# Optimization experiments

Hardware: AMD Instinct MI355X
Metric: run time of the kernel (lower is better)

Reference implementation:

```python
import jax, jax.numpy as jnp
import numpy as np

N_HEAD, D_K, D_V, D_MODEL = 16, 64, 64, 1024
LN_EPS = 1e-5


def setup_inputs() -> dict:
    key = jax.random.key(0)
    ks = jax.random.split(key, 13)
    B, S = 2, 2048
    s = 1.0 / np.sqrt(D_MODEL)
    return {
        "q": jax.random.normal(ks[0], (B, S, D_MODEL), jnp.float32),
        "k": jax.random.normal(ks[1], (B, S, D_MODEL), jnp.float32),
        "v": jax.random.normal(ks[2], (B, S, D_MODEL), jnp.float32),
        "Wq": jax.random.normal(ks[3], (D_MODEL, N_HEAD * D_K), jnp.float32) * s,
        "bq": jnp.zeros((N_HEAD * D_K,), jnp.float32),
        "Wk": jax.random.normal(ks[4], (D_MODEL, N_HEAD * D_K), jnp.float32) * s,
        "bk": jnp.zeros((N_HEAD * D_K,), jnp.float32),
        "Wv": jax.random.normal(ks[5], (D_MODEL, N_HEAD * D_V), jnp.float32) * s,
        "bv": jnp.zeros((N_HEAD * D_V,), jnp.float32),
        "Wo": jax.random.normal(ks[6], (N_HEAD * D_V, D_MODEL), jnp.float32) * s,
        "bo": jnp.zeros((D_MODEL,), jnp.float32),
        "ln_gamma": jnp.ones((D_MODEL,), jnp.float32),
        "ln_beta": jnp.zeros((D_MODEL,), jnp.float32),
    }


def reference(q, k, v, Wq, bq, Wk, bk, Wv, bv, Wo, bo, ln_gamma, ln_beta):
    B, S, _ = q.shape
    temperature = jnp.asarray(np.power(D_K, 0.5), q.dtype)
    # QKV projections -> [B, S, H, d]
    q_ = (q @ Wq + bq).reshape(B, S, N_HEAD, D_K)
    k_ = (k @ Wk + bk).reshape(B, S, N_HEAD, D_K)
    v_ = (v @ Wv + bv).reshape(B, S, N_HEAD, D_V)
    # scaled dot-product attention per head
    scores = jnp.einsum("bqhd,bkhd->bhqk", q_, k_) / temperature
    attn = jax.nn.softmax(scores, axis=-1)
    ctx = jnp.einsum("bhqk,bkhd->bqhd", attn, v_).reshape(B, S, N_HEAD * D_V)
    # output projection + residual + LayerNorm
    out = ctx @ Wo + bo + q
    mu = jnp.mean(out, axis=-1, keepdims=True)
    var = jnp.var(out, axis=-1, keepdims=True)
    out = (out - mu) * jax.lax.rsqrt(var + LN_EPS) * ln_gamma + ln_beta
    return out
```

## Files before the change

### kernel.cpp

```cpp
#include <hip/hip_runtime.h>
#include <hip/hip_bf16.h>

typedef float f32x4 __attribute__((ext_vector_type(4)));
typedef float f32x16 __attribute__((ext_vector_type(16)));
typedef __bf16 bf16x8 __attribute__((ext_vector_type(8)));
typedef __bf16 bf16x4 __attribute__((ext_vector_type(4)));
typedef unsigned u32x2 __attribute__((ext_vector_type(2)));

#define DM 1024
#define SL 2048
#define NHEAD 16
#define LOG2E 1.44269504088896f
#define EXP2(x) __builtin_amdgcn_exp2f(x)

static __device__ __forceinline__ f32x4 mfma16(bf16x8 a, bf16x8 b, f32x4 c) {
    return __builtin_amdgcn_mfma_f32_16x16x32_bf16(a, b, c, 0, 0, 0);
}
static __device__ __forceinline__ f32x16 mfma32(bf16x8 a, bf16x8 b, f32x16 c) {
    return __builtin_amdgcn_mfma_f32_32x32x16_bf16(a, b, c, 0, 0, 0);
}

static __device__ __forceinline__ void gload16(const void* g, void* l) {
    __builtin_amdgcn_global_load_lds(
        (const __attribute__((address_space(1))) unsigned*)g,
        (__attribute__((address_space(3))) unsigned*)l, 16, 0, 0);
}

static __device__ __forceinline__ unsigned packbf(float lo, float hi) {
    unsigned short lu = __builtin_bit_cast(unsigned short, (__bf16)lo);
    unsigned short hu = __builtin_bit_cast(unsigned short, (__bf16)hi);
    return ((unsigned)hu << 16) | (unsigned)lu;
}

__global__ __launch_bounds__(256) void cast_kernel(
    const float* __restrict__ x0, const float* __restrict__ x1, const float* __restrict__ x2,
    __bf16* __restrict__ y0, __bf16* __restrict__ y1, __bf16* __restrict__ y2)
{
    const float* x = (blockIdx.y == 0) ? x0 : (blockIdx.y == 1) ? x1 : x2;
    __bf16* y = (blockIdx.y == 0) ? y0 : (blockIdx.y == 1) ? y1 : y2;
    size_t i = ((size_t)blockIdx.x * 256 + threadIdx.x) * 8;
    float4 a = *reinterpret_cast<const float4*>(&x[i]);
    float4 b = *reinterpret_cast<const float4*>(&x[i + 4]);
    bf16x8 o;
    o[0] = (__bf16)a.x; o[1] = (__bf16)a.y; o[2] = (__bf16)a.z; o[3] = (__bf16)a.w;
    o[4] = (__bf16)b.x; o[5] = (__bf16)b.y; o[6] = (__bf16)b.z; o[7] = (__bf16)b.w;
    *reinterpret_cast<bf16x8*>(&y[i]) = o;
}

__global__ __launch_bounds__(256) void wt4_kernel(
    const float* __restrict__ W0, const float* __restrict__ W1,
    const float* __restrict__ W2, const float* __restrict__ W3,
    __bf16* __restrict__ T0, __bf16* __restrict__ T1,
    __bf16* __restrict__ T2, __bf16* __restrict__ T3)
{
    const float* W = (blockIdx.z == 0) ? W0 : (blockIdx.z == 1) ? W1
                   : (blockIdx.z == 2) ? W2 : W3;
    __bf16* Wt = (blockIdx.z == 0) ? T0 : (blockIdx.z == 1) ? T1
               : (blockIdx.z == 2) ? T2 : T3;
    __shared__ float tle[32][33];
    const int tx = threadIdx.x, ty = threadIdx.y;
    const int n0 = blockIdx.x * 32, k0 = blockIdx.y * 32;
#pragma unroll
    for (int i = 0; i < 4; ++i) {
        int r = ty + 8 * i;
        tle[r][tx] = W[(size_t)(k0 + r) * DM + (n0 + tx)];
    }
    __syncthreads();
#pragma unroll
    for (int i = 0; i < 4; ++i) {
        int r = ty + 8 * i;
        Wt[(size_t)(n0 + r) * DM + (k0 + tx)] = (__bf16)tle[tx][r];
    }
}

static __device__ __forceinline__ void gemm_body_bf16(
    const __bf16* __restrict__ A, const __bf16* __restrict__ Wt,
    const float* __restrict__ bias,
    __bf16* __restrict__ Yb,
    int mode, float oscale, int r0, int c0)
{
    __shared__ __attribute__((aligned(16))) __bf16 As[128 * 64];
    __shared__ __attribute__((aligned(16))) __bf16 Bs[128 * 64];
    const int t = threadIdx.x;
    const int w = t >> 6, lane = t & 63;
    const int l15 = lane & 15, lhi = lane >> 4;
    const int wr = w >> 1, wc = w & 1;
    const int lrow = lane >> 3;
    const int lcolswz = (((lane & 7) ^ lrow) << 3);
    const int jb = w * 4;
    const int swzr = (l15 & 7) << 3;

    const f32x4 fzero = {0.f, 0.f, 0.f, 0.f};
    f32x4 acc[4][4];
#pragma unroll
    for (int m = 0; m < 4; ++m)
#pragma unroll
        for (int n = 0; n < 4; ++n) acc[m][n] = fzero;

    const __bf16* gA = &A[(size_t)(r0 + jb * 8 + lrow) * DM + lcolswz];
    const __bf16* gB = &Wt[(size_t)(c0 + jb * 8 + lrow) * DM + lcolswz];

    for (int kt = 0; kt < DM; kt += 64) {
        __syncthreads();
#pragma unroll
        for (int i = 0; i < 4; ++i) {
            gload16(gA + (size_t)i * 8 * DM + kt, &As[(jb + i) * 512]);
            gload16(gB + (size_t)i * 8 * DM + kt, &Bs[(jb + i) * 512]);
        }
        __syncthreads();
#pragma unroll
        for (int kk = 0; kk < 2; ++kk) {
            bf16x8 af[4], bfr[4];
#pragma unroll
            for (int m = 0; m < 4; ++m)
                af[m] = *reinterpret_cast<const bf16x8*>(
                    &As[(wr * 64 + m * 16 + l15) * 64 + ((kk * 32 + lhi * 8) ^ swzr)]);
#pragma unroll
            for (int n = 0; n < 4; ++n)
                bfr[n] = *reinterpret_cast<const bf16x8*>(
                    &Bs[(wc * 64 + n * 16 + l15) * 64 + ((kk * 32 + lhi * 8) ^ swzr)]);
#pragma unroll
            for (int m = 0; m < 4; ++m)
#pragma unroll
                for (int n = 0; n < 4; ++n)
                    acc[m][n] = mfma16(af[m], bfr[n], acc[m][n]);
        }
    }
    if (mode == 0) {
#pragma unroll
        for (int m = 0; m < 4; ++m)
#pragma unroll
            for (int n = 0; n < 4; ++n)
#pragma unroll
                for (int r = 0; r < 4; ++r) {
                    int grow = r0 + wr * 64 + m * 16 + lhi * 4 + r;
                    int gcol = c0 + wc * 64 + n * 16 + l15;
                    Yb[(size_t)grow * DM + gcol] =
                        (__bf16)((acc[m][n][r] + bias[gcol]) * oscale);
                }
    } else {
#pragma unroll
        for (int m = 0; m < 4; ++m)
#pragma unroll
            for (int n = 0; n < 4; ++n) {
                int token = r0 + wr * 64 + m * 16 + lhi * 4;
                int gcol = c0 + wc * 64 + n * 16 + l15;
                int bb = token >> 11, ss = token & (SL - 1);
                int hh = gcol >> 6, dd = gcol & 63;
                float bv = bias[gcol];
                bf16x4 pv;
#pragma unroll
                for (int r = 0; r < 4; ++r) pv[r] = (__bf16)(acc[m][n][r] + bv);
                *reinterpret_cast<bf16x4*>(
                    &Yb[(((size_t)(bb * NHEAD + hh)) * 64 + dd) * SL + ss]) = pv;
            }
    }
}

__global__ __launch_bounds__(256) void qkv_kernel(
    const __bf16* __restrict__ xq, const __bf16* __restrict__ xk, const __bf16* __restrict__ xv,
    const __bf16* __restrict__ WtQ, const __bf16* __restrict__ WtK, const __bf16* __restrict__ WtV,
    const float* __restrict__ bq, const float* __restrict__ bk, const float* __restrict__ bv,
    __bf16* __restrict__ Qp, __bf16* __restrict__ Kp, __bf16* __restrict__ Vt)
{
    const int p = blockIdx.x;
    const int logical = (p & 7) * 96 + (p >> 3);
    const int x = logical & 7;
    const int s = logical >> 3;
    const int y = s & 31, z = s >> 5;
    const __bf16* X = (z == 0) ? xq : (z == 1) ? xk : xv;
    const __bf16* Wt = (z == 0) ? WtQ : (z == 1) ? WtK : WtV;
    const float* bias = (z == 0) ? bq : (z == 1) ? bk : bv;
    __bf16* Yb = (z == 0) ? Qp : (z == 1) ? Kp : Vt;
    int mode = (z == 2) ? 1 : 0;
    float oscale = (z == 0) ? (0.125f * LOG2E) : 1.0f;
    gemm_body_bf16(X, Wt, bias, Yb, mode, oscale, y * 128, x * 128);
}

__global__ __launch_bounds__(256) void oproj_kernel(
    const __bf16* __restrict__ Cxb, const __bf16* __restrict__ WtO,
    const float* __restrict__ bo, const float* __restrict__ resid,
    float* __restrict__ pre)
{
    __shared__ __attribute__((aligned(16))) __bf16 As[128 * 64];
    __shared__ __attribute__((aligned(16))) __bf16 Bs[64 * 64];
    const int p = blockIdx.x;
    const int logical = (p & 7) * 64 + (p >> 3);
    const int x = logical & 15, y = logical >> 4;
    const int r0 = y * 128, c0 = x * 64;

    const int t = threadIdx.x;
    const int w = t >> 6, lane = t & 63;
    const int l15 = lane & 15, lhi = lane >> 4;
    const int wr = w >> 1, wc = w & 1;
    const int lrow = lane >> 3;
    const int lcolswz = (((lane & 7) ^ lrow) << 3);
    const int jb = w * 4, jb2 = w * 2;
    const int swzr = (l15 & 7) << 3;

    const f32x4 fzero = {0.f, 0.f, 0.f, 0.f};
    f32x4 acc[4][2];
#pragma unroll
    for (int m = 0; m < 4; ++m)
#pragma unroll
        for (int n = 0; n < 2; ++n) acc[m][n] = fzero;

    const __bf16* gA = &Cxb[(size_t)(r0 + jb * 8 + lrow) * DM + lcolswz];
    const __bf16* gB = &WtO[(size_t)(c0 + jb2 * 8 + lrow) * DM + lcolswz];

    for (int kt = 0; kt < DM; kt += 64) {
        __syncthreads();
#pragma unroll
        for (int i = 0; i < 4; ++i)
            gload16(gA + (size_t)i * 8 * DM + kt, &As[(jb + i) * 512]);
#pragma unroll
        for (int i = 0; i < 2; ++i)
            gload16(gB + (size_t)i * 8 * DM + kt, &Bs[(jb2 + i) * 512]);
        __syncthreads();
#pragma unroll
        for (int kk = 0; kk < 2; ++kk) {
            bf16x8 af[4], bfr[2];
#pragma unroll
            for (int m = 0; m < 4; ++m)
                af[m] = *reinterpret_cast<const bf16x8*>(
                    &As[(wr * 64 + m * 16 + l15) * 64 + ((kk * 32 + lhi * 8) ^ swzr)]);
#pragma unroll
            for (int n = 0; n < 2; ++n)
                bfr[n] = *reinterpret_cast<const bf16x8*>(
                    &Bs[(wc * 32 + n * 16 + l15) * 64 + ((kk * 32 + lhi * 8) ^ swzr)]);
#pragma unroll
            for (int m = 0; m < 4; ++m)
#pragma unroll
                for (int n = 0; n < 2; ++n)
                    acc[m][n] = mfma16(af[m], bfr[n], acc[m][n]);
        }
    }
#pragma unroll
    for (int m = 0; m < 4; ++m)
#pragma unroll
        for (int n = 0; n < 2; ++n)
#pragma unroll
            for (int r = 0; r < 4; ++r) {
                int grow = r0 + wr * 64 + m * 16 + lhi * 4 + r;
                int gcol = c0 + wc * 32 + n * 16 + l15;
                size_t idx = (size_t)grow * DM + gcol;
                pre[idx] = acc[m][n][r] + bo[gcol] + resid[idx];
            }
}

__global__ __launch_bounds__(512, 4) void attn_kernel(
    const __bf16* __restrict__ Qp, const __bf16* __restrict__ Kp,
    const __bf16* __restrict__ Vt, __bf16* __restrict__ Op, float2* __restrict__ ML)
{
    __shared__ __attribute__((aligned(16))) __bf16 Kl[2][4096];
    __shared__ __attribute__((aligned(16))) __bf16 Vl[2][4096];
    const int t = threadIdx.x;
    const int w = t >> 6, lane = t & 63;
    const int l31 = lane & 31, hi = lane >> 5;

    const int id = blockIdx.x;
    const int logical = (id & 7) * 64 + (id >> 3);
    const int bh = logical >> 4, rr = logical & 15;
    const int qs = rr >> 1, half = rr & 1;
    const int b = bh >> 4, h = bh & 15;
    const size_t tokQ = (size_t)b * SL + qs * 256 + w * 32;
    const size_t kbase = (size_t)b * SL + half * 1024;
    const size_t vrow0 = (size_t)bh * 64;

    const int srow = t >> 3, scol = (t & 7) << 3;
    const __bf16* gK = &Kp[(kbase + srow) * DM + h * 64 + scol];
    const __bf16* gV = &Vt[(vrow0 + srow) * SL + half * 1024 + scol];
    const int sidx = ((srow * 128 + scol * 2) ^ ((srow & 7) << 4)) >> 1;

    bf16x8 bq[4];
#pragma unroll
    for (int ks = 0; ks < 4; ++ks)
        bq[ks] = *reinterpret_cast<const bf16x8*>(
            &Qp[(tokQ + l31) * DM + h * 64 + ks * 16 + hi * 8]);

    f32x16 o0, o1;
#pragma unroll
    for (int r = 0; r < 16; ++r) { o0[r] = 0.f; o1[r] = 0.f; }
    float m_run = -1e30f, l_run = 0.f;

    const int swz = (l31 & 7) << 4;
    const int NT = 1024 / 64;

    {
        bf16x8 kv = *reinterpret_cast<const bf16x8*>(gK);
        bf16x8 vv = *reinterpret_cast<const bf16x8*>(gV);
        *reinterpret_cast<bf16x8*>(&Kl[0][sidx]) = kv;
        *reinterpret_cast<bf16x8*>(&Vl[0][sidx]) = vv;
    }

    for (int ti = 0; ti < NT; ++ti) {
        const int cb = ti & 1;
        const bool pf = (ti + 1 < NT);
        bf16x8 kvn, vvn;
        if (pf) {
            kvn = *reinterpret_cast<const bf16x8*>(gK + (size_t)(ti + 1) * 64 * DM);
            vvn = *reinterpret_cast<const bf16x8*>(gV + (ti + 1) * 64);
        }
        __syncthreads();

        f32x16 c0, c1;
#pragma unroll
        for (int r = 0; r < 16; ++r) { c0[r] = 0.f; c1[r] = 0.f; }
        __builtin_amdgcn_s_setprio(1);
#pragma unroll
        for (int ks = 0; ks < 4; ++ks) {
            int off = ks * 32 + hi * 16;
            bf16x8 ak0 = *reinterpret_cast<const bf16x8*>(&Kl[cb][((l31 * 128 + off) ^ swz) >> 1]);
            bf16x8 ak1 = *reinterpret_cast<const bf16x8*>(&Kl[cb][(((32 + l31) * 128 + off) ^ swz) >> 1]);
            c0 = mfma32(ak0, bq[ks], c0);
            c1 = mfma32(ak1, bq[ks], c1);
        }
        __builtin_amdgcn_s_setprio(0);

        float mx[8];
#pragma unroll
        for (int r = 0; r < 8; ++r)
            mx[r] = fmaxf(fmaxf(c0[r], c0[r + 8]), fmaxf(c1[r], c1[r + 8]));
#pragma unroll
        for (int r = 0; r < 4; ++r) mx[r] = fmaxf(mx[r], mx[r + 4]);
        float tm = fmaxf(fmaxf(mx[0], mx[1]), fmaxf(mx[2], mx[3]));
        tm = fmaxf(tm, __shfl_xor(tm, 32));

        if (__any(tm > m_run + 11.5f)) {
            float nm = fmaxf(m_run, tm);
            float sc = EXP2(m_run - nm);
            m_run = nm;
            l_run *= sc;
#pragma unroll
            for (int r = 0; r < 16; ++r) {
                float sq = __shfl(sc, (r & 3) + 8 * (r >> 2) + 4 * hi);
                o0[r] *= sq; o1[r] *= sq;
            }
        }

        float s4a = 0.f, s4b = 0.f, s4c = 0.f, s4d = 0.f;
#pragma unroll
        for (int r = 0; r < 16; r += 4) {
            c0[r]     = EXP2(c0[r]     - m_run); s4a += c0[r];
            c0[r + 1] = EXP2(c0[r + 1] - m_run); s4b += c0[r + 1];
            c0[r + 2] = EXP2(c0[r + 2] - m_run); s4c += c0[r + 2];
            c0[r + 3] = EXP2(c0[r + 3] - m_run); s4d += c0[r + 3];
        }
#pragma unroll
        for (int r = 0; r < 16; r += 4) {
            c1[r]     = EXP2(c1[r]     - m_run); s4a += c1[r];
            c1[r + 1] = EXP2(c1[r + 1] - m_run); s4b += c1[r + 1];
            c1[r + 2] = EXP2(c1[r + 2] - m_run); s4c += c1[r + 2];
            c1[r + 3] = EXP2(c1[r + 3] - m_run); s4d += c1[r + 3];
        }
        float rs = (s4a + s4b) + (s4c + s4d);
        rs += __shfl_xor(rs, 32);
        l_run += rs;

        if (pf) {
            *reinterpret_cast<bf16x8*>(&Kl[cb ^ 1][sidx]) = kvn;
            *reinterpret_cast<bf16x8*>(&Vl[cb ^ 1][sidx]) = vvn;
        }

        unsigned wd0[8], wd1[8];
#pragma unroll
        for (int tt = 0; tt < 4; ++tt)
#pragma unroll
            for (int p = 0; p < 2; ++p) {
                wd0[tt * 2 + p] = packbf(c0[4 * tt + 2 * p], c0[4 * tt + 2 * p + 1]);
                wd1[tt * 2 + p] = packbf(c1[4 * tt + 2 * p], c1[4 * tt + 2 * p + 1]);
            }
        unsigned ua[4][4];
#pragma unroll
        for (int s = 0; s < 4; ++s) {
            int tA = (s & 1) * 2;
#pragma unroll
            for (int p = 0; p < 2; ++p) {
                unsigned va = (s < 2) ? wd0[tA * 2 + p] : wd1[tA * 2 + p];
                unsigned vb = (s < 2) ? wd0[(tA + 1) * 2 + p] : wd1[(tA + 1) * 2 + p];
                u32x2 rres = __builtin_amdgcn_permlane32_swap(va, vb, false, false);
                ua[s][p] = rres[0]; ua[s][2 + p] = rres[1];
            }
        }

        __builtin_amdgcn_s_setprio(1);
#pragma unroll
        for (int s = 0; s < 4; ++s) {
            bf16x8 as = *reinterpret_cast<const bf16x8*>(&ua[s][0]);
            bf16x8 vf0 = *reinterpret_cast<const bf16x8*>(
                &Vl[cb][((l31 * 128 + s * 32 + hi * 16) ^ swz) >> 1]);
            bf16x8 vf1 = *reinterpret_cast<const bf16x8*>(
                &Vl[cb][(((32 + l31) * 128 + s * 32 + hi * 16) ^ swz) >> 1]);
            o0 = mfma32(as, vf0, o0);
            o1 = mfma32(as, vf1, o1);
        }
        __builtin_amdgcn_s_setprio(0);
    }

    if (hi == 0)
        ML[((size_t)half * 4096 + tokQ + l31) * NHEAD + h] = float2{m_run, l_run};
    const size_t obase = (size_t)half * 4096 * DM;
#pragma unroll
    for (int r = 0; r < 16; ++r) {
        int qq = (r & 3) + 8 * (r >> 2) + 4 * hi;
        size_t rowi = obase + (tokQ + qq) * DM + h * 64;
        Op[rowi + l31]      = (__bf16)o0[r];
        Op[rowi + 32 + l31] = (__bf16)o1[r];
    }
}

__global__ __launch_bounds__(256) void combine_kernel(
    const __bf16* __restrict__ Op, const float2* __restrict__ ML,
    __bf16* __restrict__ Cxb)
{
    const size_t e = ((size_t)blockIdx.x * 256 + threadIdx.x) * 8;
    const int token = (int)(e >> 10);
    const int h = (int)((e >> 6) & 15);
    float2 ml0 = ML[(size_t)token * NHEAD + h];
    float2 ml1 = ML[((size_t)4096 + token) * NHEAD + h];
    float M = fmaxf(ml0.x, ml1.x);
    float s0 = EXP2(ml0.x - M), s1 = EXP2(ml1.x - M);
    float inv = 1.f / (ml0.y * s0 + ml1.y * s1);
    s0 *= inv; s1 *= inv;
    bf16x8 a0 = *reinterpret_cast<const bf16x8*>(&Op[e]);
    bf16x8 a1 = *reinterpret_cast<const bf16x8*>(&Op[(size_t)4096 * DM + e]);
    bf16x8 o;
#pragma unroll
    for (int j = 0; j < 8; ++j)
        o[j] = (__bf16)((float)a0[j] * s0 + (float)a1[j] * s1);
    *reinterpret_cast<bf16x8*>(&Cxb[e]) = o;
}

__global__ __launch_bounds__(256) void ln_kernel(
    const float* __restrict__ X, const float* __restrict__ gamma,
    const float* __restrict__ beta, float* __restrict__ out)
{
    const int row = blockIdx.x, t = threadIdx.x;
    float4 v = *reinterpret_cast<const float4*>(&X[(size_t)row * DM + t * 4]);
    float s = v.x + v.y + v.z + v.w;
    float s2 = v.x * v.x + v.y * v.y + v.z * v.z + v.w * v.w;
#pragma unroll
    for (int off = 1; off < 64; off <<= 1) {
        s += __shfl_xor(s, off);
        s2 += __shfl_xor(s2, off);
    }
    __shared__ float rs[4], rs2[4];
    const int w = t >> 6;
    if ((t & 63) == 0) { rs[w] = s; rs2[w] = s2; }
    __syncthreads();
    s = rs[0] + rs[1] + rs[2] + rs[3];
    s2 = rs2[0] + rs2[1] + rs2[2] + rs2[3];
    float mean = s * (1.f / DM);
    float var = s2 * (1.f / DM) - mean * mean;
    float rstd = rsqrtf(var + 1e-5f);
    int c = t * 4;
    float4 o;
    o.x = (v.x - mean) * rstd * gamma[c + 0] + beta[c + 0];
    o.y = (v.y - mean) * rstd * gamma[c + 1] + beta[c + 1];
    o.z = (v.z - mean) * rstd * gamma[c + 2] + beta[c + 2];
    o.w = (v.w - mean) * rstd * gamma[c + 3] + beta[c + 3];
    *reinterpret_cast<float4*>(&out[(size_t)row * DM + c]) = o;
}

extern "C" void kernel_launch(void* const* d_in, const int* in_sizes, int n_in,
                              void* d_out, int out_size, void* d_ws, size_t ws_size,
                              hipStream_t stream) {
    (void)in_sizes; (void)n_in; (void)out_size; (void)ws_size;
    const float* q   = (const float*)d_in[0];
    const float* k   = (const float*)d_in[1];
    const float* v   = (const float*)d_in[2];
    const float* Wq  = (const float*)d_in[3];
    const float* bq  = (const float*)d_in[4];
    const float* Wk  = (const float*)d_in[5];
    const float* bk  = (const float*)d_in[6];
    const float* Wv  = (const float*)d_in[7];
    const float* bv  = (const float*)d_in[8];
    const float* Wo  = (const float*)d_in[9];
    const float* bo  = (const float*)d_in[10];
    const float* lng = (const float*)d_in[11];
    const float* lnb = (const float*)d_in[12];

    char* ws = (char*)d_ws;
    const size_t MB = (size_t)1 << 20;
    __bf16* WtQ = (__bf16*)(ws + 0 * MB);
    __bf16* WtK = (__bf16*)(ws + 2 * MB);
    __bf16* WtV = (__bf16*)(ws + 4 * MB);
    __bf16* WtO = (__bf16*)(ws + 6 * MB);
    __bf16* Xbq = (__bf16*)(ws + 8 * MB);
    __bf16* Xbk = (__bf16*)(ws + 16 * MB);
    __bf16* Xbv = (__bf16*)(ws + 24 * MB);
    __bf16* Qp  = (__bf16*)(ws + 32 * MB);
    __bf16* Kp  = (__bf16*)(ws + 40 * MB);
    __bf16* Vt  = (__bf16*)(ws + 48 * MB);
    __bf16* Cxb = (__bf16*)(ws + 56 * MB);
    __bf16* Op  = (__bf16*)(ws + 8 * MB);
    float2* ML  = (float2*)(ws + 24 * MB);
    float*  pre = (float*)(ws + 8 * MB);

    cast_kernel<<<dim3(2048, 3), 256, 0, stream>>>(q, k, v, Xbq, Xbk, Xbv);
    wt4_kernel<<<dim3(32, 32, 4), dim3(32, 8), 0, stream>>>(
        Wq, Wk, Wv, Wo, WtQ, WtK, WtV, WtO);

    qkv_kernel<<<dim3(768), 256, 0, stream>>>(Xbq, Xbk, Xbv, WtQ, WtK, WtV,
                                              bq, bk, bv, Qp, Kp, Vt);
    attn_kernel<<<dim3(512), 512, 0, stream>>>(Qp, Kp, Vt, Op, ML);
    combine_kernel<<<dim3(2048), 256, 0, stream>>>(Op, ML, Cxb);
    oproj_kernel<<<dim3(512), 256, 0, stream>>>(Cxb, WtO, bo, q, pre);
    ln_kernel<<<4096, 256, 0, stream>>>(pre, lng, lnb, (float*)d_out);
}
```

Before: 147.6 us.

## Merge prep kernels, shrink QKV GEMM tiles, halve attention block size

Fuses the input cast and weight transpose into a single prep launch. The QKV projection now reuses the 128x64 GEMM body shared with the output projection, so it runs twice as many blocks. Attention blocks drop from 512 to 256 threads (128 query rows each), with every thread loading two K/V rows per tile, which doubles the grid to 1024 blocks. The aim is more blocks to fill the CUs and one fewer launch, at the cost of less operand reuse per block and more redundant K/V loading across blocks.

```diff
diff --git a/kernel.cpp b/kernel.cpp
--- a/kernel.cpp
+++ b/kernel.cpp
@@ -32,163 +32,57 @@
     return ((unsigned)hu << 16) | (unsigned)lu;
 }
 
-__global__ __launch_bounds__(256) void cast_kernel(
+__global__ __launch_bounds__(256) void prep_kernel(
     const float* __restrict__ x0, const float* __restrict__ x1, const float* __restrict__ x2,
-    __bf16* __restrict__ y0, __bf16* __restrict__ y1, __bf16* __restrict__ y2)
-{
-    const float* x = (blockIdx.y == 0) ? x0 : (blockIdx.y == 1) ? x1 : x2;
-    __bf16* y = (blockIdx.y == 0) ? y0 : (blockIdx.y == 1) ? y1 : y2;
-    size_t i = ((size_t)blockIdx.x * 256 + threadIdx.x) * 8;
-    float4 a = *reinterpret_cast<const float4*>(&x[i]);
-    float4 b = *reinterpret_cast<const float4*>(&x[i + 4]);
-    bf16x8 o;
-    o[0] = (__bf16)a.x; o[1] = (__bf16)a.y; o[2] = (__bf16)a.z; o[3] = (__bf16)a.w;
-    o[4] = (__bf16)b.x; o[5] = (__bf16)b.y; o[6] = (__bf16)b.z; o[7] = (__bf16)b.w;
-    *reinterpret_cast<bf16x8*>(&y[i]) = o;
-}
-
-__global__ __launch_bounds__(256) void wt4_kernel(
+    __bf16* __restrict__ y0, __bf16* __restrict__ y1, __bf16* __restrict__ y2,
     const float* __restrict__ W0, const float* __restrict__ W1,
     const float* __restrict__ W2, const float* __restrict__ W3,
     __bf16* __restrict__ T0, __bf16* __restrict__ T1,
     __bf16* __restrict__ T2, __bf16* __restrict__ T3)
 {
-    const float* W = (blockIdx.z == 0) ? W0 : (blockIdx.z == 1) ? W1
-                   : (blockIdx.z == 2) ? W2 : W3;
-    __bf16* Wt = (blockIdx.z == 0) ? T0 : (blockIdx.z == 1) ? T1
-               : (blockIdx.z == 2) ? T2 : T3;
-    __shared__ float tle[32][33];
-    const int tx = threadIdx.x, ty = threadIdx.y;
-    const int n0 = blockIdx.x * 32, k0 = blockIdx.y * 32;
-#pragma unroll
-    for (int i = 0; i < 4; ++i) {
-        int r = ty + 8 * i;
-        tle[r][tx] = W[(size_t)(k0 + r) * DM + (n0 + tx)];
-    }
-    __syncthreads();
-#pragma unroll
-    for (int i = 0; i < 4; ++i) {
-        int r = ty + 8 * i;
-        Wt[(size_t)(n0 + r) * DM + (k0 + tx)] = (__bf16)tle[tx][r];
-    }
-}
-
-static __device__ __forceinline__ void gemm_body_bf16(
+    const int bid = blockIdx.x;
+    if (bid < 6144) {
+        const int yy = bid >> 11, xx = bid & 2047;
+        const float* x = (yy == 0) ? x0 : (yy == 1) ? x1 : x2;
+        __bf16* y = (yy == 0) ? y0 : (yy == 1) ? y1 : y2;
+        size_t i = ((size_t)xx * 256 + threadIdx.x) * 8;
+        float4 a = *reinterpret_cast<const float4*>(&x[i]);
+        float4 b = *reinterpret_cast<const float4*>(&x[i + 4]);
+        bf16x8 o;
+        o[0] = (__bf16)a.x; o[1] = (__bf16)a.y; o[2] = (__bf16)a.z; o[3] = (__bf16)a.w;
+        o[4] = (__bf16)b.x; o[5] = (__bf16)b.y; o[6] = (__bf16)b.z; o[7] = (__bf16)b.w;
+        *reinterpret_cast<bf16x8*>(&y[i]) = o;
+    } else {
+        __shared__ float tle[32][33];
+        const int rem = bid - 6144;
+        const int z = rem >> 10, r2 = rem & 1023;
+        const int bx = r2 & 31, by = r2 >> 5;
+        const float* W = (z == 0) ? W0 : (z == 1) ? W1 : (z == 2) ? W2 : W3;
+        __bf16* Wt = (z == 0) ? T0 : (z == 1) ? T1 : (z == 2) ? T2 : T3;
+        const int tx = threadIdx.x & 31, ty = threadIdx.x >> 5;
+        const int n0 = bx * 32, k0 = by * 32;
+#pragma unroll
+        for (int i = 0; i < 4; ++i) {
+            int r = ty + 8 * i;
+            tle[r][tx] = W[(size_t)(k0 + r) * DM + (n0 + tx)];
+        }
+        __syncthreads();
+#pragma unroll
+        for (int i = 0; i < 4; ++i) {
+            int r = ty + 8 * i;
+            Wt[(size_t)(n0 + r) * DM + (k0 + tx)] = (__bf16)tle[tx][r];
+        }
+    }
+}
+
+static __device__ __forceinline__ void gemm64_body(
     const __bf16* __restrict__ A, const __bf16* __restrict__ Wt,
-    const float* __restrict__ bias,
-    __bf16* __restrict__ Yb,
+    const float* __restrict__ bias, const float* __restrict__ resid,
+    __bf16* __restrict__ Yb, float* __restrict__ Yf,
     int mode, float oscale, int r0, int c0)
-{
-    __shared__ __attribute__((aligned(16))) __bf16 As[128 * 64];
-    __shared__ __attribute__((aligned(16))) __bf16 Bs[128 * 64];
-    const int t = threadIdx.x;
-    const int w = t >> 6, lane = t & 63;
-    const int l15 = lane & 15, lhi = lane >> 4;
-    const int wr = w >> 1, wc = w & 1;
-    const int lrow = lane >> 3;
-    const int lcolswz = (((lane & 7) ^ lrow) << 3);
-    const int jb = w * 4;
-    const int swzr = (l15 & 7) << 3;
-
-    const f32x4 fzero = {0.f, 0.f, 0.f, 0.f};
-    f32x4 acc[4][4];
-#pragma unroll
-    for (int m = 0; m < 4; ++m)
-#pragma unroll
-        for (int n = 0; n < 4; ++n) acc[m][n] = fzero;
-
-    const __bf16* gA = &A[(size_t)(r0 + jb * 8 + lrow) * DM + lcolswz];
-    const __bf16* gB = &Wt[(size_t)(c0 + jb * 8 + lrow) * DM + lcolswz];
-
-    for (int kt = 0; kt < DM; kt += 64) {
-        __syncthreads();
-#pragma unroll
-        for (int i = 0; i < 4; ++i) {
-            gload16(gA + (size_t)i * 8 * DM + kt, &As[(jb + i) * 512]);
-            gload16(gB + (size_t)i * 8 * DM + kt, &Bs[(jb + i) * 512]);
-        }
-        __syncthreads();
-#pragma unroll
-        for (int kk = 0; kk < 2; ++kk) {
-            bf16x8 af[4], bfr[4];
-#pragma unroll
-            for (int m = 0; m < 4; ++m)
-                af[m] = *reinterpret_cast<const bf16x8*>(
-                    &As[(wr * 64 + m * 16 + l15) * 64 + ((kk * 32 + lhi * 8) ^ swzr)]);
-#pragma unroll
-            for (int n = 0; n < 4; ++n)
-                bfr[n] = *reinterpret_cast<const bf16x8*>(
-                    &Bs[(wc * 64 + n * 16 + l15) * 64 + ((kk * 32 + lhi * 8) ^ swzr)]);
-#pragma unroll
-            for (int m = 0; m < 4; ++m)
-#pragma unroll
-                for (int n = 0; n < 4; ++n)
-                    acc[m][n] = mfma16(af[m], bfr[n], acc[m][n]);
-        }
-    }
-    if (mode == 0) {
-#pragma unroll
-        for (int m = 0; m < 4; ++m)
-#pragma unroll
-            for (int n = 0; n < 4; ++n)
-#pragma unroll
-                for (int r = 0; r < 4; ++r) {
-                    int grow = r0 + wr * 64 + m * 16 + lhi * 4 + r;
-                    int gcol = c0 + wc * 64 + n * 16 + l15;
-                    Yb[(size_t)grow * DM + gcol] =
-                        (__bf16)((acc[m][n][r] + bias[gcol]) * oscale);
-                }
-    } else {
-#pragma unroll
-        for (int m = 0; m < 4; ++m)
-#pragma unroll
-            for (int n = 0; n < 4; ++n) {
-                int token = r0 + wr * 64 + m * 16 + lhi * 4;
-                int gcol = c0 + wc * 64 + n * 16 + l15;
-                int bb = token >> 11, ss = token & (SL - 1);
-                int hh = gcol >> 6, dd = gcol & 63;
-                float bv = bias[gcol];
-                bf16x4 pv;
-#pragma unroll
-                for (int r = 0; r < 4; ++r) pv[r] = (__bf16)(acc[m][n][r] + bv);
-                *reinterpret_cast<bf16x4*>(
-                    &Yb[(((size_t)(bb * NHEAD + hh)) * 64 + dd) * SL + ss]) = pv;
-            }
-    }
-}
-
-__global__ __launch_bounds__(256) void qkv_kernel(
-    const __bf16* __restrict__ xq, const __bf16* __restrict__ xk, const __bf16* __restrict__ xv,
-    const __bf16* __restrict__ WtQ, const __bf16* __restrict__ WtK, const __bf16* __restrict__ WtV,
-    const float* __restrict__ bq, const float* __restrict__ bk, const float* __restrict__ bv,
-    __bf16* __restrict__ Qp, __bf16* __restrict__ Kp, __bf16* __restrict__ Vt)
-{
-    const int p = blockIdx.x;
-    const int logical = (p & 7) * 96 + (p >> 3);
-    const int x = logical & 7;
-    const int s = logical >> 3;
-    const int y = s & 31, z = s >> 5;
-    const __bf16* X = (z == 0) ? xq : (z == 1) ? xk : xv;
-    const __bf16* Wt = (z == 0) ? WtQ : (z == 1) ? WtK : WtV;
-    const float* bias = (z == 0) ? bq : (z == 1) ? bk : bv;
-    __bf16* Yb = (z == 0) ? Qp : (z == 1) ? Kp : Vt;
-    int mode = (z == 2) ? 1 : 0;
-    float oscale = (z == 0) ? (0.125f * LOG2E) : 1.0f;
-    gemm_body_bf16(X, Wt, bias, Yb, mode, oscale, y * 128, x * 128);
-}
-
-__global__ __launch_bounds__(256) void oproj_kernel(
-    const __bf16* __restrict__ Cxb, const __bf16* __restrict__ WtO,
-    const float* __restrict__ bo, const float* __restrict__ resid,
-    float* __restrict__ pre)
 {
     __shared__ __attribute__((aligned(16))) __bf16 As[128 * 64];
     __shared__ __attribute__((aligned(16))) __bf16 Bs[64 * 64];
-    const int p = blockIdx.x;
-    const int logical = (p & 7) * 64 + (p >> 3);
-    const int x = logical & 15, y = logical >> 4;
-    const int r0 = y * 128, c0 = x * 64;
-
     const int t = threadIdx.x;
     const int w = t >> 6, lane = t & 63;
     const int l15 = lane & 15, lhi = lane >> 4;
@@ -205,8 +99,8 @@
 #pragma unroll
         for (int n = 0; n < 2; ++n) acc[m][n] = fzero;
 
-    const __bf16* gA = &Cxb[(size_t)(r0 + jb * 8 + lrow) * DM + lcolswz];
-    const __bf16* gB = &WtO[(size_t)(c0 + jb2 * 8 + lrow) * DM + lcolswz];
+    const __bf16* gA = &A[(size_t)(r0 + jb * 8 + lrow) * DM + lcolswz];
+    const __bf16* gB = &Wt[(size_t)(c0 + jb2 * 8 + lrow) * DM + lcolswz];
 
     for (int kt = 0; kt < DM; kt += 64) {
         __syncthreads();
@@ -235,20 +129,81 @@
                     acc[m][n] = mfma16(af[m], bfr[n], acc[m][n]);
         }
     }
-#pragma unroll
-    for (int m = 0; m < 4; ++m)
-#pragma unroll
-        for (int n = 0; n < 2; ++n)
-#pragma unroll
-            for (int r = 0; r < 4; ++r) {
-                int grow = r0 + wr * 64 + m * 16 + lhi * 4 + r;
+    if (mode == 0) {
+#pragma unroll
+        for (int m = 0; m < 4; ++m)
+#pragma unroll
+            for (int n = 0; n < 2; ++n)
+#pragma unroll
+                for (int r = 0; r < 4; ++r) {
+                    int grow = r0 + wr * 64 + m * 16 + lhi * 4 + r;
+                    int gcol = c0 + wc * 32 + n * 16 + l15;
+                    Yb[(size_t)grow * DM + gcol] =
+                        (__bf16)((acc[m][n][r] + bias[gcol]) * oscale);
+                }
+    } else if (mode == 1) {
+#pragma unroll
+        for (int m = 0; m < 4; ++m)
+#pragma unroll
+            for (int n = 0; n < 2; ++n) {
+                int token = r0 + wr * 64 + m * 16 + lhi * 4;
                 int gcol = c0 + wc * 32 + n * 16 + l15;
-                size_t idx = (size_t)grow * DM + gcol;
-                pre[idx] = acc[m][n][r] + bo[gcol] + resid[idx];
+                int bb = token >> 11, ss = token & (SL - 1);
+                int hh = gcol >> 6, dd = gcol & 63;
+                float bv = bias[gcol];
+                bf16x4 pv;
+#pragma unroll
+                for (int r = 0; r < 4; ++r) pv[r] = (__bf16)(acc[m][n][r] + bv);
+                *reinterpret_cast<bf16x4*>(
+                    &Yb[(((size_t)(bb * NHEAD + hh)) * 64 + dd) * SL + ss]) = pv;
             }
-}
-
-__global__ __launch_bounds__(512, 4) void attn_kernel(
+    } else {
+#pragma unroll
+        for (int m = 0; m < 4; ++m)
+#pragma unroll
+            for (int n = 0; n < 2; ++n)
+#pragma unroll
+                for (int r = 0; r < 4; ++r) {
+                    int grow = r0 + wr * 64 + m * 16 + lhi * 4 + r;
+                    int gcol = c0 + wc * 32 + n * 16 + l15;
+                    size_t idx = (size_t)grow * DM + gcol;
+                    Yf[idx] = acc[m][n][r] + bias[gcol] + resid[idx];
+                }
+    }
+}
+
+__global__ __launch_bounds__(256) void qkv_kernel(
+    const __bf16* __restrict__ xq, const __bf16* __restrict__ xk, const __bf16* __restrict__ xv,
+    const __bf16* __restrict__ WtQ, const __bf16* __restrict__ WtK, const __bf16* __restrict__ WtV,
+    const float* __restrict__ bq, const float* __restrict__ bk, const float* __restrict__ bv,
+    __bf16* __restrict__ Qp, __bf16* __restrict__ Kp, __bf16* __restrict__ Vt)
+{
+    const int p = blockIdx.x;
+    const int logical = (p & 7) * 192 + (p >> 3);
+    const int x = logical & 15;
+    const int s = logical >> 4;
+    const int y = s & 31, z = s >> 5;
+    const __bf16* X = (z == 0) ? xq : (z == 1) ? xk : xv;
+    const __bf16* Wt = (z == 0) ? WtQ : (z == 1) ? WtK : WtV;
+    const float* bias = (z == 0) ? bq : (z == 1) ? bk : bv;
+    __bf16* Yb = (z == 0) ? Qp : (z == 1) ? Kp : Vt;
+    int mode = (z == 2) ? 1 : 0;
+    float oscale = (z == 0) ? (0.125f * LOG2E) : 1.0f;
+    gemm64_body(X, Wt, bias, nullptr, Yb, nullptr, mode, oscale, y * 128, x * 64);
+}
+
+__global__ __launch_bounds__(256) void oproj_kernel(
+    const __bf16* __restrict__ Cxb, const __bf16* __restrict__ WtO,
+    const float* __restrict__ bo, const float* __restrict__ resid,
+    float* __restrict__ pre)
+{
+    const int p = blockIdx.x;
+    const int logical = (p & 7) * 64 + (p >> 3);
+    const int x = logical & 15, y = logical >> 4;
+    gemm64_body(Cxb, WtO, bo, resid, nullptr, pre, 2, 1.0f, y * 128, x * 64);
+}
+
+__global__ __launch_bounds__(256, 4) void attn_kernel(
     const __bf16* __restrict__ Qp, const __bf16* __restrict__ Kp,
     const __bf16* __restrict__ Vt, __bf16* __restrict__ Op, float2* __restrict__ ML)
 {
@@ -259,18 +214,19 @@
     const int l31 = lane & 31, hi = lane >> 5;
 
     const int id = blockIdx.x;
-    const int logical = (id & 7) * 64 + (id >> 3);
-    const int bh = logical >> 4, rr = logical & 15;
+    const int logical = (id & 7) * 128 + (id >> 3);
+    const int bh = logical >> 5, rr = logical & 31;
     const int qs = rr >> 1, half = rr & 1;
     const int b = bh >> 4, h = bh & 15;
-    const size_t tokQ = (size_t)b * SL + qs * 256 + w * 32;
+    const size_t tokQ = (size_t)b * SL + qs * 128 + w * 32;
     const size_t kbase = (size_t)b * SL + half * 1024;
     const size_t vrow0 = (size_t)bh * 64;
 
     const int srow = t >> 3, scol = (t & 7) << 3;
     const __bf16* gK = &Kp[(kbase + srow) * DM + h * 64 + scol];
     const __bf16* gV = &Vt[(vrow0 + srow) * SL + half * 1024 + scol];
-    const int sidx = ((srow * 128 + scol * 2) ^ ((srow & 7) << 4)) >> 1;
+    const int sidxA = ((srow * 128 + scol * 2) ^ ((srow & 7) << 4)) >> 1;
+    const int sidxB = sidxA + 2048;
 
     bf16x8 bq[4];
 #pragma unroll
@@ -287,19 +243,23 @@
     const int NT = 1024 / 64;
 
     {
-        bf16x8 kv = *reinterpret_cast<const bf16x8*>(gK);
-        bf16x8 vv = *reinterpret_cast<const bf16x8*>(gV);
-        *reinterpret_cast<bf16x8*>(&Kl[0][sidx]) = kv;
-        *reinterpret_cast<bf16x8*>(&Vl[0][sidx]) = vv;
+        *reinterpret_cast<bf16x8*>(&Kl[0][sidxA]) = *reinterpret_cast<const bf16x8*>(gK);
+        *reinterpret_cast<bf16x8*>(&Kl[0][sidxB]) = *reinterpret_cast<const bf16x8*>(gK + (size_t)32 * DM);
+        *reinterpret_cast<bf16x8*>(&Vl[0][sidxA]) = *reinterpret_cast<const bf16x8*>(gV);
+        *reinterpret_cast<bf16x8*>(&Vl[0][sidxB]) = *reinterpret_cast<const bf16x8*>(gV + (size_t)32 * SL);
     }
 
     for (int ti = 0; ti < NT; ++ti) {
         const int cb = ti & 1;
         const bool pf = (ti + 1 < NT);
-        bf16x8 kvn, vvn;
+        bf16x8 kvnA, kvnB, vvnA, vvnB;
         if (pf) {
-            kvn = *reinterpret_cast<const bf16x8*>(gK + (size_t)(ti + 1) * 64 * DM);
-            vvn = *reinterpret_cast<const bf16x8*>(gV + (ti + 1) * 64);
+            const __bf16* nK = gK + (size_t)(ti + 1) * 64 * DM;
+            const __bf16* nV = gV + (ti + 1) * 64;
+            kvnA = *reinterpret_cast<const bf16x8*>(nK);
+            kvnB = *reinterpret_cast<const bf16x8*>(nK + (size_t)32 * DM);
+            vvnA = *reinterpret_cast<const bf16x8*>(nV);
+            vvnB = *reinterpret_cast<const bf16x8*>(nV + (size_t)32 * SL);
         }
         __syncthreads();
 
@@ -358,8 +318,10 @@
         l_run += rs;
 
         if (pf) {
-            *reinterpret_cast<bf16x8*>(&Kl[cb ^ 1][sidx]) = kvn;
-            *reinterpret_cast<bf16x8*>(&Vl[cb ^ 1][sidx]) = vvn;
+            *reinterpret_cast<bf16x8*>(&Kl[cb ^ 1][sidxA]) = kvnA;
+            *reinterpret_cast<bf16x8*>(&Kl[cb ^ 1][sidxB]) = kvnB;
+            *reinterpret_cast<bf16x8*>(&Vl[cb ^ 1][sidxA]) = vvnA;
+            *reinterpret_cast<bf16x8*>(&Vl[cb ^ 1][sidxB]) = vvnB;
         }
 
         unsigned wd0[8], wd1[8];
@@ -497,13 +459,12 @@
     float2* ML  = (float2*)(ws + 24 * MB);
     float*  pre = (float*)(ws + 8 * MB);
 
-    cast_kernel<<<dim3(2048, 3), 256, 0, stream>>>(q, k, v, Xbq, Xbk, Xbv);
-    wt4_kernel<<<dim3(32, 32, 4), dim3(32, 8), 0, stream>>>(
-        Wq, Wk, Wv, Wo, WtQ, WtK, WtV, WtO);
-
-    qkv_kernel<<<dim3(768), 256, 0, stream>>>(Xbq, Xbk, Xbv, WtQ, WtK, WtV,
-                                              bq, bk, bv, Qp, Kp, Vt);
-    attn_kernel<<<dim3(512), 512, 0, stream>>>(Qp, Kp, Vt, Op, ML);
+    prep_kernel<<<dim3(10240), 256, 0, stream>>>(q, k, v, Xbq, Xbk, Xbv,
+                                                 Wq, Wk, Wv, Wo, WtQ, WtK, WtV, WtO);
+
+    qkv_kernel<<<dim3(1536), 256, 0, stream>>>(Xbq, Xbk, Xbv, WtQ, WtK, WtV,
+                                               bq, bk, bv, Qp, Kp, Vt);
+    attn_kernel<<<dim3(1024), 256, 0, stream>>>(Qp, Kp, Vt, Op, ML);
     combine_kernel<<<dim3(2048), 256, 0, stream>>>(Op, ML, Cxb);
     oproj_kernel<<<dim3(512), 256, 0, stream>>>(Cxb, WtO, bo, q, pre);
     ln_kernel<<<4096, 256, 0, stream>>>(pre, lng, lnb, (float*)d_out);
```

New measurement: 146.1 us. No clear change (-1.0%).
